# Kernel tuning notes

Measured on AMD Instinct MI355X. Metric: run time of the kernel, lower is better.

Reference implementation:

```python
import jax, jax.numpy as jnp
import numpy as np

EPS = 1e-8
NUM_ITER = 3
NUM_SLOTS = 8
NUM_HEADS = 4


def _ln(x, w, b):
    m = x.mean(-1, keepdims=True)
    v = x.var(-1, keepdims=True)
    return (x - m) / jnp.sqrt(v + 1e-5) * w + b


def setup_inputs() -> dict:
    key = jax.random.key(0)
    B, T, N, D, S, H = 16, 12, 1024, 256, 128, 256
    K = NUM_SLOTS
    ks = jax.random.split(key, 32)
    w = lambda i, shape: (0.02 * jax.random.normal(ks[i], shape)).astype(jnp.float32)
    f32 = jnp.float32
    return {
        'inputs': jax.random.normal(ks[0], (B, T, N, D), f32),
        'slots_noise': jax.random.normal(ks[1], (B, K, S), f32),
        'slot_mu': w(2, (1, 1, S)),
        'slot_log_sigma': w(3, (1, 1, S)),
        'ln_in_w': jnp.ones((D,), f32), 'ln_in_b': jnp.zeros((D,), f32),
        'ln_slots_w': jnp.ones((S,), f32), 'ln_slots_b': jnp.zeros((S,), f32),
        'ln_mlp_w': jnp.ones((S,), f32), 'ln_mlp_b': jnp.zeros((S,), f32),
        'Wq': w(4, (S, S)), 'Wk': w(5, (D, S)), 'Wv': w(6, (D, S)),
        'gru_Wih': w(7, (3 * S, S)), 'gru_Whh': w(8, (3 * S, S)),
        'gru_bih': jnp.zeros((3 * S,), f32), 'gru_bhh': jnp.zeros((3 * S,), f32),
        'mlp_W1': w(9, (S, H)), 'mlp_b1': jnp.zeros((H,), f32),
        'mlp_W2': w(10, (H, S)), 'mlp_b2': jnp.zeros((S,), f32),
        'p_ln1_w': jnp.ones((S,), f32), 'p_ln1_b': jnp.zeros((S,), f32),
        'p_Wq': w(11, (S, S)), 'p_Wk': w(12, (S, S)), 'p_Wv': w(13, (S, S)), 'p_Wo': w(14, (S, S)),
        'p_ln2_w': jnp.ones((S,), f32), 'p_ln2_b': jnp.zeros((S,), f32),
        'p_ffn_W1': w(15, (S, 4 * S)), 'p_ffn_b1': jnp.zeros((4 * S,), f32),
        'p_ffn_W2': w(16, (4 * S, S)), 'p_ffn_b2': jnp.zeros((S,), f32),
        'p_lnf_w': jnp.ones((S,), f32), 'p_lnf_b': jnp.zeros((S,), f32),
    }


def reference(inputs, slots_noise, slot_mu, slot_log_sigma,
              ln_in_w, ln_in_b, ln_slots_w, ln_slots_b, ln_mlp_w, ln_mlp_b,
              Wq, Wk, Wv, gru_Wih, gru_Whh, gru_bih, gru_bhh,
              mlp_W1, mlp_b1, mlp_W2, mlp_b2,
              p_ln1_w, p_ln1_b, p_Wq, p_Wk, p_Wv, p_Wo,
              p_ln2_w, p_ln2_b, p_ffn_W1, p_ffn_b1, p_ffn_W2, p_ffn_b2,
              p_lnf_w, p_lnf_b):
    B, T, N, D = inputs.shape
    S = slot_mu.shape[-1]
    K = NUM_SLOTS

    slots0 = slot_mu + jnp.exp(slot_log_sigma) * slots_noise  # (B,K,S)
    x = _ln(inputs, ln_in_w, ln_in_b)
    k = (x @ Wk) * (S ** -0.5)  # (B,T,N,S), pre-scaled keys
    v = x @ Wv                  # (B,T,N,S)

    def gru(u, h):  # torch GRUCell semantics; u,h: (B*K,S)
        gi = u @ gru_Wih.T + gru_bih
        gh = h @ gru_Whh.T + gru_bhh
        i_r, i_z, i_n = jnp.split(gi, 3, -1)
        h_r, h_z, h_n = jnp.split(gh, 3, -1)
        r = jax.nn.sigmoid(i_r + h_r)
        z = jax.nn.sigmoid(i_z + h_z)
        n = jnp.tanh(i_n + r * h_n)
        return (1.0 - z) * n + z * h

    def mha(y):  # (B,K,S) self-attention, pre-LN block style
        dh = S // NUM_HEADS
        split = lambda t: t.reshape(B, K, NUM_HEADS, dh).transpose(0, 2, 1, 3)
        q = split(y @ p_Wq) * (dh ** -0.5)
        kk = split(y @ p_Wk)
        vv = split(y @ p_Wv)
        a = jax.nn.softmax(jnp.einsum('bhqd,bhkd->bhqk', q, kk), -1)
        o = jnp.einsum('bhqk,bhkd->bhqd', a, vv).transpose(0, 2, 1, 3).reshape(B, K, S)
        return o @ p_Wo

    def predictor(s):
        s = s + mha(_ln(s, p_ln1_w, p_ln1_b))
        h = _ln(s, p_ln2_w, p_ln2_b)
        s = s + (jax.nn.relu(h @ p_ffn_W1 + p_ffn_b1) @ p_ffn_W2 + p_ffn_b2)
        return _ln(s, p_lnf_w, p_lnf_b)

    def step(slots, kv_t):
        k_t, v_t = kv_t  # (B,N,S) each
        attn_vis = None
        for i in range(NUM_ITER):
            slots_prev = slots
            q = _ln(slots, ln_slots_w, ln_slots_b) @ Wq          # (B,K,S)
            logits = jnp.einsum('bns,bks->bnk', k_t, q)           # (B,N,K)
            attn_vis = jax.nn.softmax(logits, -1)                 # over slots
            attn = attn_vis + EPS
            attn = attn / attn.sum(1, keepdims=True)              # normalize over inputs
            updates = jnp.einsum('bnk,bns->bks', attn, v_t)       # (B,K,S)
            slots = gru(updates.reshape(-1, S), slots_prev.reshape(-1, S)).reshape(B, K, S)
            if i < NUM_ITER - 1:
                h = _ln(slots, ln_mlp_w, ln_mlp_b)
                slots = slots + (jax.nn.relu(h @ mlp_W1 + mlp_b1) @ mlp_W2 + mlp_b2)
        return predictor(slots), (slots, attn_vis)

    kT = jnp.swapaxes(k, 0, 1)  # (T,B,N,S)
    vT = jnp.swapaxes(v, 0, 1)
    _, (slots_seq, attn_seq) = jax.lax.scan(step, slots0, (kT, vT))
    slots_collect = jnp.swapaxes(slots_seq, 0, 1)  # (B,T,K,S)
    attns_collect = jnp.swapaxes(attn_seq, 0, 1)   # (B,T,N,K)
    return slots_collect, attns_collect
```

## Files before the change

### kernel.cpp

```cpp
#include <hip/hip_runtime.h>
#include <hip/hip_bf16.h>

typedef _Float16 half8 __attribute__((ext_vector_type(8)));
typedef float floatx4 __attribute__((ext_vector_type(4)));

#define MFMA_F16(a, b, c) __builtin_amdgcn_mfma_f32_16x16x32_f16((a), (b), (c), 0, 0, 0)

__global__ void prep_w_kernel(const float* __restrict__ src, _Float16* __restrict__ dst,
                              int In, int Out, float scale, int doT) {
  int idx = blockIdx.x * 256 + threadIdx.x;
  if (idx >= In * Out) return;
  float v;
  if (doT) { int o = idx / In, i = idx - o * In; v = src[i * Out + o]; }
  else     { v = src[idx]; }
  dst[idx] = (_Float16)(v * scale);
}

__global__ void init_ctr_kernel(int* __restrict__ ctr) {
  if (threadIdx.x < 16) ctr[threadIdx.x] = 0;
}

__global__ __launch_bounds__(256) void gemm_kv_kernel(
    const float* __restrict__ x, const float* __restrict__ lnw_g,
    const float* __restrict__ lnb_g, const _Float16* __restrict__ WT,
    _Float16* __restrict__ kout, _Float16* __restrict__ vTout) {
  __shared__ union {
    struct { _Float16 A[128][72]; _Float16 B[128][72]; } s;
    _Float16 C[128][136];
  } u;
  __shared__ float s_mean[128], s_rstd[128], s_red[256][2], s_lnw[256], s_lnb[256];

  const int tid = threadIdx.x;
  const int bx = blockIdx.x, y = blockIdx.y;
  const size_t r0 = (size_t)bx * 128;
  const int w = tid >> 6, lane = tid & 63, quad = lane >> 4, l15 = lane & 15;

  s_lnw[tid] = lnw_g[tid];
  s_lnb[tid] = lnb_g[tid];
  {
    int row = tid >> 1, half = tid & 1;
    const float* p = x + (r0 + row) * 256 + half * 128;
    float s = 0.f, sq = 0.f;
    for (int i = 0; i < 32; i++) {
      float4 d = ((const float4*)p)[i];
      s += d.x + d.y + d.z + d.w;
      sq += d.x * d.x + d.y * d.y + d.z * d.z + d.w * d.w;
    }
    s_red[tid][0] = s; s_red[tid][1] = sq;
  }
  __syncthreads();
  if (tid < 128) {
    float s  = s_red[2 * tid][0] + s_red[2 * tid + 1][0];
    float sq = s_red[2 * tid][1] + s_red[2 * tid + 1][1];
    float m = s * (1.f / 256.f);
    float v = sq * (1.f / 256.f) - m * m;
    s_mean[tid] = m; s_rstd[tid] = rsqrtf(v + 1e-5f);
  }

  floatx4 acc[2][8];
  for (int rt = 0; rt < 2; rt++)
    for (int ct = 0; ct < 8; ct++) acc[rt][ct] = (floatx4){0.f, 0.f, 0.f, 0.f};

  for (int c = 0; c < 4; c++) {
    __syncthreads();
    for (int i = 0; i < 4; i++) {
      int g = tid + 256 * i;
      int row = g >> 3, c8 = g & 7;
      int col0 = c * 64 + c8 * 8;
      const float* p = x + (r0 + row) * 256 + col0;
      float4 d0 = ((const float4*)p)[0];
      float4 d1 = ((const float4*)p)[1];
      float f[8] = {d0.x, d0.y, d0.z, d0.w, d1.x, d1.y, d1.z, d1.w};
      float m = s_mean[row], rs = s_rstd[row];
      half8 hv;
      #pragma unroll
      for (int j = 0; j < 8; j++)
        hv[j] = (_Float16)((f[j] - m) * rs * s_lnw[col0 + j] + s_lnb[col0 + j]);
      *(half8*)&u.s.A[row][c8 * 8] = hv;
      *(half8*)&u.s.B[row][c8 * 8] = *(const half8*)(WT + (size_t)(y * 128 + row) * 256 + col0);
    }
    __syncthreads();
    #pragma unroll
    for (int ks = 0; ks < 2; ks++) {
      half8 af[2];
      af[0] = *(const half8*)&u.s.A[(2 * w) * 16 + l15][ks * 32 + quad * 8];
      af[1] = *(const half8*)&u.s.A[(2 * w + 1) * 16 + l15][ks * 32 + quad * 8];
      #pragma unroll
      for (int ct = 0; ct < 8; ct++) {
        half8 bf = *(const half8*)&u.s.B[ct * 16 + l15][ks * 32 + quad * 8];
        acc[0][ct] = MFMA_F16(af[0], bf, acc[0][ct]);
        acc[1][ct] = MFMA_F16(af[1], bf, acc[1][ct]);
      }
    }
  }

  const size_t bt = (size_t)(bx >> 3);
  const int n0loc = (bx & 7) * 128;
  if (y == 0) {
    for (int rt = 0; rt < 2; rt++)
      for (int ct = 0; ct < 8; ct++)
        #pragma unroll
        for (int r = 0; r < 4; r++) {
          size_t row = r0 + (2 * w + rt) * 16 + quad * 4 + r;
          kout[row * 128 + ct * 16 + l15] = (_Float16)acc[rt][ct][r];
        }
  } else {
    __syncthreads();
    for (int rt = 0; rt < 2; rt++)
      for (int ct = 0; ct < 8; ct++)
        #pragma unroll
        for (int r = 0; r < 4; r++)
          u.C[(2 * w + rt) * 16 + quad * 4 + r][ct * 16 + l15] = (_Float16)acc[rt][ct][r];
    __syncthreads();
    int s = tid >> 1, hf = tid & 1;
    for (int j = 0; j < 8; j++) {
      int nb = hf * 64 + j * 8;
      half8 tmp;
      #pragma unroll
      for (int e = 0; e < 8; e++) tmp[e] = u.C[nb + e][s];
      *(half8*)(vTout + (bt * 128 + s) * 1024 + n0loc + nb) = tmp;
    }
  }
}

struct P2Args {
  const _Float16 *kbuf, *vT;
  const _Float16 *WqT, *Wih, *Whh, *W1T, *W2T;
  const _Float16 *pQT, *pKT, *pVT, *pOT, *pF1T, *pF2T;
  const float *noise, *mu, *lsig;
  const float *lnsw, *lnsb, *lnmw, *lnmb;
  const float *bih, *bhh, *mb1, *mb2;
  const float *pl1w, *pl1b, *pl2w, *pl2b, *fb1, *fb2, *plfw, *plfb;
  float *out_slots, *out_attn;
  float *upd_p;
  float *col_p;
  float *vs_p;
  int   *ctr;
};

struct SH {
  _Float16 k_lds[128][136];
  _Float16 v_lds[128][136];
  float slots[8][128];
  _Float16 a16[16][136];
  _Float16 h16[16][136];
  union {
    struct { _Float16 qT[16][136]; _Float16 attnT[16][136]; } sa;
    struct { float gi[8][384]; float gh[8][384]; } gru;
    struct { _Float16 m16[16][264]; } mlp;
    struct { float qh[8][128]; float kh[8][128]; float vh[8][128]; float sc[4][8][8]; } mha;
    struct { _Float16 f16[16][520]; } ffn;
  } u;
  float colsum[8];
  float vsum[128];
  float bih[384], bhh[384], mb1[256], mb2[128], fb1[512], fb2[128];
  float lnsw[128], lnsb[128], lnmw[128], lnmb[128];
  float pl1w[128], pl1b[128], pl2w[128], pl2b[128], plfw[128], plfb[128];
};

__device__ __forceinline__ void group_barrier(int* ctr, int target) {
  __syncthreads();
  if (threadIdx.x == 0) {
    __hip_atomic_fetch_add(ctr, 1, __ATOMIC_ACQ_REL, __HIP_MEMORY_SCOPE_AGENT);
    while (__hip_atomic_load(ctr, __ATOMIC_ACQUIRE, __HIP_MEMORY_SCOPE_AGENT) < target)
      __builtin_amdgcn_s_sleep(1);
  }
  __syncthreads();
}

__device__ __forceinline__ void ln_to_a16(SH* sh, const float (*src)[128],
                                          const float* wv, const float* bv,
                                          int w, int lane) {
  if (w < 8) {
    float x0 = src[w][lane], x1 = src[w][lane + 64];
    float s = x0 + x1, sq = x0 * x0 + x1 * x1;
    #pragma unroll
    for (int m = 1; m < 64; m <<= 1) { s += __shfl_xor(s, m); sq += __shfl_xor(sq, m); }
    float mn = s * 0.0078125f;
    float vr = sq * 0.0078125f - mn * mn;
    float rs = rsqrtf(vr + 1e-5f);
    sh->a16[w][lane]      = (_Float16)((x0 - mn) * rs * wv[lane]      + bv[lane]);
    sh->a16[w][lane + 64] = (_Float16)((x1 - mn) * rs * wv[lane + 64] + bv[lane + 64]);
  } else {
    sh->a16[w][lane] = (_Float16)0.f;
    sh->a16[w][lane + 64] = (_Float16)0.f;
  }
}

__global__ __launch_bounds__(1024) void slot_attn_kernel(P2Args P) {
  __shared__ SH sh;
  const int tid = threadIdx.x;
  const int w = tid >> 6, lane = tid & 63, quad = lane >> 4, l15 = lane & 15;
  const int b = blockIdx.x & 15;
  const int g = blockIdx.x >> 4;
  const int n0 = g * 128;
  int* ctrb = P.ctr + b;
  int bar_phase = 0;

  for (int i = tid; i < 384; i += 1024) { sh.bih[i] = P.bih[i]; sh.bhh[i] = P.bhh[i]; }
  for (int i = tid; i < 256; i += 1024) sh.mb1[i] = P.mb1[i];
  for (int i = tid; i < 512; i += 1024) sh.fb1[i] = P.fb1[i];
  if (tid < 128) {
    sh.mb2[tid]  = P.mb2[tid];  sh.fb2[tid]  = P.fb2[tid];
    sh.lnsw[tid] = P.lnsw[tid]; sh.lnsb[tid] = P.lnsb[tid];
    sh.lnmw[tid] = P.lnmw[tid]; sh.lnmb[tid] = P.lnmb[tid];
    sh.pl1w[tid] = P.pl1w[tid]; sh.pl1b[tid] = P.pl1b[tid];
    sh.pl2w[tid] = P.pl2w[tid]; sh.pl2b[tid] = P.pl2b[tid];
    sh.plfw[tid] = P.plfw[tid]; sh.plfb[tid] = P.plfb[tid];
  }
  {
    int kk = tid >> 7, s = tid & 127;
    sh.slots[kk][s] = P.mu[s] + expf(P.lsig[s]) * P.noise[(b * 8 + kk) * 128 + s];
  }
  __syncthreads();

  for (int t = 0; t < 12; t++) {
    const _Float16* kt = P.kbuf + ((size_t)(b * 12 + t)) * 1024 * 128 + (size_t)n0 * 128;
    const _Float16* vt = P.vT   + ((size_t)(b * 12 + t)) * 128 * 1024 + n0;
    {
      int r = tid >> 4, c8 = (tid & 15) * 8;
      #pragma unroll
      for (int p = 0; p < 2; p++) {
        int row = p * 64 + r;
        *(half8*)&sh.k_lds[row][c8] = *(const half8*)(kt + (size_t)row * 128 + c8);
        *(half8*)&sh.v_lds[row][c8] = *(const half8*)(vt + (size_t)row * 1024 + c8);
      }
    }
    if (tid < 128) sh.vsum[tid] = 0.f;
    __syncthreads();
    {
      int s = tid >> 3, j = tid & 7;
      float a = 0.f;
      #pragma unroll
      for (int e = 0; e < 16; e++) a += (float)sh.v_lds[s][j * 16 + e];
      atomicAdd(&sh.vsum[s], a);
    }
    __syncthreads();
    if (tid < 128)
      __hip_atomic_store(&P.vs_p[(b * 8 + g) * 128 + tid], sh.vsum[tid],
                         __ATOMIC_RELAXED, __HIP_MEMORY_SCOPE_AGENT);

    for (int it = 0; it < 3; it++) {
      const int par = (t * 3 + it) & 1;
      float* updg = P.upd_p + ((size_t)(par * 16 + b) * 8 + g) * 1024;
      float* colg = P.col_p + ((size_t)(par * 16 + b) * 8 + g) * 8;
      if (w < 8) {
        float x0 = sh.slots[w][lane], x1 = sh.slots[w][lane + 64];
        sh.h16[w][lane] = (_Float16)x0; sh.h16[w][lane + 64] = (_Float16)x1;
        float s = x0 + x1, sq = x0 * x0 + x1 * x1;
        #pragma unroll
        for (int m = 1; m < 64; m <<= 1) { s += __shfl_xor(s, m); sq += __shfl_xor(sq, m); }
        float mn = s * 0.0078125f;
        float vr = sq * 0.0078125f - mn * mn;
        float rs = rsqrtf(vr + 1e-5f);
        sh.a16[w][lane]      = (_Float16)((x0 - mn) * rs * sh.lnsw[lane]      + sh.lnsb[lane]);
        sh.a16[w][lane + 64] = (_Float16)((x1 - mn) * rs * sh.lnsw[lane + 64] + sh.lnsb[lane + 64]);
      } else {
        sh.h16[w][lane] = (_Float16)0.f; sh.h16[w][lane + 64] = (_Float16)0.f;
        sh.a16[w][lane] = (_Float16)0.f; sh.a16[w][lane + 64] = (_Float16)0.f;
      }
      if (tid < 8) sh.colsum[tid] = 0.f;
      __syncthreads();
      if (w < 8) {
        floatx4 acc = (floatx4){0.f, 0.f, 0.f, 0.f};
        const _Float16* ar = &sh.a16[l15][quad * 8];
        const _Float16* br = P.WqT + (size_t)(w * 16 + l15) * 128 + quad * 8;
        #pragma unroll
        for (int ks = 0; ks < 4; ks++)
          acc = MFMA_F16(*(const half8*)(ar + ks * 32), *(const half8*)(br + ks * 32), acc);
        #pragma unroll
        for (int r = 0; r < 4; r++)
          sh.u.sa.qT[quad * 4 + r][w * 16 + l15] = (_Float16)acc[r];
      }
      __syncthreads();
      if (w < 8) {
        int nloc0 = w * 16;
        floatx4 acc = (floatx4){0.f, 0.f, 0.f, 0.f};
        const _Float16* ar = &sh.k_lds[nloc0 + l15][quad * 8];
        const _Float16* br = &sh.u.sa.qT[l15][quad * 8];
        #pragma unroll
        for (int ks = 0; ks < 4; ks++)
          acc = MFMA_F16(*(const half8*)(ar + ks * 32), *(const half8*)(br + ks * 32), acc);
        float cs = 0.f;
        #pragma unroll
        for (int r = 0; r < 4; r++) {
          float v = (l15 < 8) ? acc[r] : -3.0e38f;
          float mx = v;
          mx = fmaxf(mx, __shfl_xor(mx, 1, 16));
          mx = fmaxf(mx, __shfl_xor(mx, 2, 16));
          mx = fmaxf(mx, __shfl_xor(mx, 4, 16));
          mx = fmaxf(mx, __shfl_xor(mx, 8, 16));
          float pv = (l15 < 8) ? expf(v - mx) : 0.f;
          float ss = pv;
          ss += __shfl_xor(ss, 1, 16); ss += __shfl_xor(ss, 2, 16);
          ss += __shfl_xor(ss, 4, 16); ss += __shfl_xor(ss, 8, 16);
          float pn = pv / ss;
          cs += pn;
          int nloc = nloc0 + quad * 4 + r;
          sh.u.sa.attnT[l15][nloc] = (_Float16)pn;
          if (it == 2 && l15 < 8)
            P.out_attn[((size_t)(b * 12 + t) * 1024 + n0 + nloc) * 8 + l15] = pn;
        }
        cs += __shfl_xor(cs, 16); cs += __shfl_xor(cs, 32);
        if (lane < 8) atomicAdd(&sh.colsum[lane], cs);
      }
      __syncthreads();
      if (w < 8) {
        floatx4 acc = (floatx4){0.f, 0.f, 0.f, 0.f};
        const _Float16* ar = &sh.u.sa.attnT[l15][quad * 8];
        const _Float16* br = &sh.v_lds[w * 16 + l15][quad * 8];
        #pragma unroll
        for (int ks = 0; ks < 4; ks++)
          acc = MFMA_F16(*(const half8*)(ar + ks * 32), *(const half8*)(br + ks * 32), acc);
        int scol = w * 16 + l15;
        #pragma unroll
        for (int r = 0; r < 4; r++) {
          int slot = quad * 4 + r;
          if (slot < 8)
            __hip_atomic_store(&updg[slot * 128 + scol], acc[r],
                               __ATOMIC_RELAXED, __HIP_MEMORY_SCOPE_AGENT);
        }
      }
      if (tid < 8)
        __hip_atomic_store(&colg[tid], sh.colsum[tid],
                           __ATOMIC_RELAXED, __HIP_MEMORY_SCOPE_AGENT);
      bar_phase++;
      group_barrier(ctrb, 8 * bar_phase);
      {
        int slot = tid >> 7, scol = tid & 127;
        const float* up = P.upd_p + (size_t)(par * 16 + b) * 8 * 1024 + slot * 128 + scol;
        float sum = 0.f;
        #pragma unroll
        for (int gg = 0; gg < 8; gg++)
          sum += __hip_atomic_load((float*)(up + gg * 1024),
                                   __ATOMIC_RELAXED, __HIP_MEMORY_SCOPE_AGENT);
        float csum = 0.f;
        if (tid < 8) {
          const float* cp = P.col_p + (size_t)(par * 16 + b) * 8 * 8 + tid;
          #pragma unroll
          for (int gg = 0; gg < 8; gg++)
            csum += __hip_atomic_load((float*)(cp + gg * 8),
                                      __ATOMIC_RELAXED, __HIP_MEMORY_SCOPE_AGENT);
        }
        float vtot = 0.f;
        if (it == 0 && tid < 128) {
          const float* vp = P.vs_p + b * 8 * 128 + tid;
          #pragma unroll
          for (int gg = 0; gg < 8; gg++)
            vtot += __hip_atomic_load((float*)(vp + gg * 128),
                                      __ATOMIC_RELAXED, __HIP_MEMORY_SCOPE_AGENT);
        }
        __syncthreads();
        if (tid < 8) sh.colsum[tid] = csum;
        if (it == 0 && tid < 128) sh.vsum[tid] = vtot;
        __syncthreads();
        float upd = (sum + 1e-8f * sh.vsum[scol]) / (sh.colsum[slot] + 1024.f * 1e-8f);
        sh.a16[slot][scol] = (_Float16)upd;
        sh.a16[slot + 8][scol] = (_Float16)0.f;
      }
      __syncthreads();
      for (int j = w; j < 48; j += 16) {
        int isGi = (j < 24) ? 1 : 0;
        int ct = isGi ? j : j - 24;
        const _Float16* Ap = isGi ? &sh.a16[0][0] : &sh.h16[0][0];
        const _Float16* Bg = (isGi ? P.Wih : P.Whh) + (size_t)(ct * 16 + l15) * 128 + quad * 8;
        const _Float16* ar = Ap + l15 * 136 + quad * 8;
        floatx4 acc = (floatx4){0.f, 0.f, 0.f, 0.f};
        #pragma unroll
        for (int ks = 0; ks < 4; ks++)
          acc = MFMA_F16(*(const half8*)(ar + ks * 32), *(const half8*)(Bg + ks * 32), acc);
        int col = ct * 16 + l15;
        float bias = isGi ? sh.bih[col] : sh.bhh[col];
        float* dst = isGi ? &sh.u.gru.gi[0][0] : &sh.u.gru.gh[0][0];
        #pragma unroll
        for (int r = 0; r < 4; r++) {
          int slot = quad * 4 + r;
          if (slot < 8) dst[slot * 384 + col] = acc[r] + bias;
        }
      }
      __syncthreads();
      {
        int kk = tid >> 7, s = tid & 127;
        float gr = sh.u.gru.gi[kk][s]       + sh.u.gru.gh[kk][s];
        float gz = sh.u.gru.gi[kk][128 + s] + sh.u.gru.gh[kk][128 + s];
        float rg = 1.f / (1.f + expf(-gr));
        float zg = 1.f / (1.f + expf(-gz));
        float ng = tanhf(sh.u.gru.gi[kk][256 + s] + rg * sh.u.gru.gh[kk][256 + s]);
        float h = sh.slots[kk][s];
        sh.slots[kk][s] = (1.f - zg) * ng + zg * h;
      }
      __syncthreads();
      if (it < 2) {
        ln_to_a16(&sh, sh.slots, sh.lnmw, sh.lnmb, w, lane);
        __syncthreads();
        {
          floatx4 acc = (floatx4){0.f, 0.f, 0.f, 0.f};
          const _Float16* ar = &sh.a16[l15][quad * 8];
          const _Float16* br = P.W1T + (size_t)(w * 16 + l15) * 128 + quad * 8;
          #pragma unroll
          for (int ks = 0; ks < 4; ks++)
            acc = MFMA_F16(*(const half8*)(ar + ks * 32), *(const half8*)(br + ks * 32), acc);
          int col = w * 16 + l15;
          #pragma unroll
          for (int r = 0; r < 4; r++) {
            int slot = quad * 4 + r;
            if (slot < 8) sh.u.mlp.m16[slot][col] = (_Float16)fmaxf(acc[r] + sh.mb1[col], 0.f);
            else          sh.u.mlp.m16[slot][col] = (_Float16)0.f;
          }
        }
        __syncthreads();
        if (w < 8) {
          floatx4 acc = (floatx4){0.f, 0.f, 0.f, 0.f};
          const _Float16* ar = &sh.u.mlp.m16[l15][quad * 8];
          const _Float16* br = P.W2T + (size_t)(w * 16 + l15) * 256 + quad * 8;
          #pragma unroll
          for (int ks = 0; ks < 8; ks++)
            acc = MFMA_F16(*(const half8*)(ar + ks * 32), *(const half8*)(br + ks * 32), acc);
          int col = w * 16 + l15;
          #pragma unroll
          for (int r = 0; r < 4; r++) {
            int slot = quad * 4 + r;
            if (slot < 8) sh.slots[slot][col] += acc[r] + sh.mb2[col];
          }
        }
        __syncthreads();
      }
    }

    if (g == 0) {
      int kk = tid >> 7, s = tid & 127;
      P.out_slots[((size_t)(b * 12 + t) * 8 + kk) * 128 + s] = sh.slots[kk][s];
    }
    ln_to_a16(&sh, sh.slots, sh.pl1w, sh.pl1b, w, lane);
    __syncthreads();
    for (int j = w; j < 24; j += 16) {
      int gg = j >> 3, ct = j & 7;
      const _Float16* Bg = (gg == 0 ? P.pQT : (gg == 1 ? P.pKT : P.pVT)) + (size_t)(ct * 16 + l15) * 128 + quad * 8;
      const _Float16* ar = &sh.a16[l15][quad * 8];
      floatx4 acc = (floatx4){0.f, 0.f, 0.f, 0.f};
      #pragma unroll
      for (int ks = 0; ks < 4; ks++)
        acc = MFMA_F16(*(const half8*)(ar + ks * 32), *(const half8*)(Bg + ks * 32), acc);
      float scale = (gg == 0) ? 0.17677669529663687f : 1.f;
      float* dst = (gg == 0 ? &sh.u.mha.qh[0][0] : (gg == 1 ? &sh.u.mha.kh[0][0] : &sh.u.mha.vh[0][0]));
      int col = ct * 16 + l15;
      #pragma unroll
      for (int r = 0; r < 4; r++) {
        int slot = quad * 4 + r;
        if (slot < 8) dst[slot * 128 + col] = acc[r] * scale;
      }
    }
    __syncthreads();
    if (tid < 256) {
      int h = tid >> 6, a = (tid >> 3) & 7, b2 = tid & 7;
      const float* qr = &sh.u.mha.qh[a][h * 32];
      const float* kr = &sh.u.mha.kh[b2][h * 32];
      float s = 0.f;
      #pragma unroll
      for (int d = 0; d < 32; d++) s += qr[d] * kr[d];
      sh.u.mha.sc[h][a][b2] = s;
    }
    __syncthreads();
    if (tid < 32) {
      int h = tid >> 3, a = tid & 7;
      float* p = sh.u.mha.sc[h][a];
      float mx = p[0];
      #pragma unroll
      for (int j = 1; j < 8; j++) mx = fmaxf(mx, p[j]);
      float e[8]; float ssum = 0.f;
      #pragma unroll
      for (int j = 0; j < 8; j++) { e[j] = expf(p[j] - mx); ssum += e[j]; }
      float inv = 1.f / ssum;
      #pragma unroll
      for (int j = 0; j < 8; j++) p[j] = e[j] * inv;
    }
    __syncthreads();
    {
      int a = tid >> 7, col = tid & 127, h = col >> 5;
      float acc = 0.f;
      #pragma unroll
      for (int b2 = 0; b2 < 8; b2++) acc += sh.u.mha.sc[h][a][b2] * sh.u.mha.vh[b2][col];
      sh.a16[a][col] = (_Float16)acc;
    }
    __syncthreads();
    if (w < 8) {
      floatx4 acc = (floatx4){0.f, 0.f, 0.f, 0.f};
      const _Float16* ar = &sh.a16[l15][quad * 8];
      const _Float16* br = P.pOT + (size_t)(w * 16 + l15) * 128 + quad * 8;
      #pragma unroll
      for (int ks = 0; ks < 4; ks++)
        acc = MFMA_F16(*(const half8*)(ar + ks * 32), *(const half8*)(br + ks * 32), acc);
      int col = w * 16 + l15;
      #pragma unroll
      for (int r = 0; r < 4; r++) {
        int slot = quad * 4 + r;
        if (slot < 8) sh.slots[slot][col] += acc[r];
      }
    }
    __syncthreads();
    ln_to_a16(&sh, sh.slots, sh.pl2w, sh.pl2b, w, lane);
    __syncthreads();
    for (int ct = w; ct < 32; ct += 16) {
      floatx4 acc = (floatx4){0.f, 0.f, 0.f, 0.f};
      const _Float16* ar = &sh.a16[l15][quad * 8];
      const _Float16* br = P.pF1T + (size_t)(ct * 16 + l15) * 128 + quad * 8;
      #pragma unroll
      for (int ks = 0; ks < 4; ks++)
        acc = MFMA_F16(*(const half8*)(ar + ks * 32), *(const half8*)(br + ks * 32), acc);
      int col = ct * 16 + l15;
      #pragma unroll
      for (int r = 0; r < 4; r++) {
        int slot = quad * 4 + r;
        if (slot < 8) sh.u.ffn.f16[slot][col] = (_Float16)fmaxf(acc[r] + sh.fb1[col], 0.f);
        else          sh.u.ffn.f16[slot][col] = (_Float16)0.f;
      }
    }
    __syncthreads();
    if (w < 8) {
      floatx4 acc = (floatx4){0.f, 0.f, 0.f, 0.f};
      const _Float16* ar = &sh.u.ffn.f16[l15][quad * 8];
      const _Float16* br = P.pF2T + (size_t)(w * 16 + l15) * 512 + quad * 8;
      #pragma unroll 4
      for (int ks = 0; ks < 16; ks++)
        acc = MFMA_F16(*(const half8*)(ar + ks * 32), *(const half8*)(br + ks * 32), acc);
      int col = w * 16 + l15;
      #pragma unroll
      for (int r = 0; r < 4; r++) {
        int slot = quad * 4 + r;
        if (slot < 8) sh.slots[slot][col] += acc[r] + sh.fb2[col];
      }
    }
    __syncthreads();
    if (w < 8) {
      float x0 = sh.slots[w][lane], x1 = sh.slots[w][lane + 64];
      float s = x0 + x1, sq = x0 * x0 + x1 * x1;
      #pragma unroll
      for (int m = 1; m < 64; m <<= 1) { s += __shfl_xor(s, m); sq += __shfl_xor(sq, m); }
      float mn = s * 0.0078125f;
      float vr = sq * 0.0078125f - mn * mn;
      float rs = rsqrtf(vr + 1e-5f);
      sh.slots[w][lane]      = (x0 - mn) * rs * sh.plfw[lane]      + sh.plfb[lane];
      sh.slots[w][lane + 64] = (x1 - mn) * rs * sh.plfw[lane + 64] + sh.plfb[lane + 64];
    }
    __syncthreads();
  }
}

extern "C" void kernel_launch(void* const* d_in, const int* in_sizes, int n_in,
                              void* d_out, int out_size, void* d_ws, size_t ws_size,
                              hipStream_t stream) {
  const float* inp   = (const float*)d_in[0];
  const float* noise = (const float*)d_in[1];
  const float* mu    = (const float*)d_in[2];
  const float* lsig  = (const float*)d_in[3];
  const float* lniw  = (const float*)d_in[4];
  const float* lnib  = (const float*)d_in[5];
  const float* lnsw  = (const float*)d_in[6];
  const float* lnsb  = (const float*)d_in[7];
  const float* lnmw  = (const float*)d_in[8];
  const float* lnmb  = (const float*)d_in[9];
  const float* Wq    = (const float*)d_in[10];
  const float* Wk    = (const float*)d_in[11];
  const float* Wv    = (const float*)d_in[12];
  const float* gWih  = (const float*)d_in[13];
  const float* gWhh  = (const float*)d_in[14];
  const float* gbih  = (const float*)d_in[15];
  const float* gbhh  = (const float*)d_in[16];
  const float* mW1   = (const float*)d_in[17];
  const float* mb1   = (const float*)d_in[18];
  const float* mW2   = (const float*)d_in[19];
  const float* mb2   = (const float*)d_in[20];
  const float* pl1w  = (const float*)d_in[21];
  const float* pl1b  = (const float*)d_in[22];
  const float* pWq   = (const float*)d_in[23];
  const float* pWk   = (const float*)d_in[24];
  const float* pWv   = (const float*)d_in[25];
  const float* pWo   = (const float*)d_in[26];
  const float* pl2w  = (const float*)d_in[27];
  const float* pl2b  = (const float*)d_in[28];
  const float* pf1   = (const float*)d_in[29];
  const float* pfb1  = (const float*)d_in[30];
  const float* pf2   = (const float*)d_in[31];
  const float* pfb2  = (const float*)d_in[32];
  const float* plfw  = (const float*)d_in[33];
  const float* plfb  = (const float*)d_in[34];

  _Float16* p   = (_Float16*)d_ws;
  _Float16* kbuf = p;  p += 25165824;
  _Float16* vT   = p;  p += 25165824;
  _Float16* WT   = p;  p += 65536;
  _Float16* WqT  = p;  p += 16384;
  _Float16* Wih  = p;  p += 49152;
  _Float16* Whh  = p;  p += 49152;
  _Float16* W1T  = p;  p += 32768;
  _Float16* W2T  = p;  p += 32768;
  _Float16* pQT  = p;  p += 16384;
  _Float16* pKT  = p;  p += 16384;
  _Float16* pVT  = p;  p += 16384;
  _Float16* pOT  = p;  p += 16384;
  _Float16* pF1T = p;  p += 65536;
  _Float16* pF2T = p;  p += 65536;
  float* fb   = (float*)p;
  float* upd_p = fb;  fb += 2 * 16 * 8 * 1024;
  float* col_p = fb;  fb += 2 * 16 * 8 * 8;
  float* vs_p  = fb;  fb += 16 * 8 * 128;
  int*   ctr   = (int*)fb;

  const float kscale = 0.08838834764831845f;
  init_ctr_kernel<<<1, 64, 0, stream>>>(ctr);
  prep_w_kernel<<<128, 256, 0, stream>>>(Wk,   WT,         256, 128, kscale, 1);
  prep_w_kernel<<<128, 256, 0, stream>>>(Wv,   WT + 32768, 256, 128, 1.f,    1);
  prep_w_kernel<<<64,  256, 0, stream>>>(Wq,   WqT,        128, 128, 1.f,    1);
  prep_w_kernel<<<192, 256, 0, stream>>>(gWih, Wih,        49152, 1, 1.f,    0);
  prep_w_kernel<<<192, 256, 0, stream>>>(gWhh, Whh,        49152, 1, 1.f,    0);
  prep_w_kernel<<<128, 256, 0, stream>>>(mW1,  W1T,        128, 256, 1.f,    1);
  prep_w_kernel<<<128, 256, 0, stream>>>(mW2,  W2T,        256, 128, 1.f,    1);
  prep_w_kernel<<<64,  256, 0, stream>>>(pWq,  pQT,        128, 128, 1.f,    1);
  prep_w_kernel<<<64,  256, 0, stream>>>(pWk,  pKT,        128, 128, 1.f,    1);
  prep_w_kernel<<<64,  256, 0, stream>>>(pWv,  pVT,        128, 128, 1.f,    1);
  prep_w_kernel<<<64,  256, 0, stream>>>(pWo,  pOT,        128, 128, 1.f,    1);
  prep_w_kernel<<<256, 256, 0, stream>>>(pf1,  pF1T,       128, 512, 1.f,    1);
  prep_w_kernel<<<256, 256, 0, stream>>>(pf2,  pF2T,       512, 128, 1.f,    1);

  dim3 g1(1536, 2, 1);
  gemm_kv_kernel<<<g1, 256, 0, stream>>>(inp, lniw, lnib, WT, kbuf, vT);

  P2Args a;
  a.kbuf = kbuf; a.vT = vT;
  a.WqT = WqT; a.Wih = Wih; a.Whh = Whh; a.W1T = W1T; a.W2T = W2T;
  a.pQT = pQT; a.pKT = pKT; a.pVT = pVT; a.pOT = pOT; a.pF1T = pF1T; a.pF2T = pF2T;
  a.noise = noise; a.mu = mu; a.lsig = lsig;
  a.lnsw = lnsw; a.lnsb = lnsb; a.lnmw = lnmw; a.lnmb = lnmb;
  a.bih = gbih; a.bhh = gbhh; a.mb1 = mb1; a.mb2 = mb2;
  a.pl1w = pl1w; a.pl1b = pl1b; a.pl2w = pl2w; a.pl2b = pl2b;
  a.fb1 = pfb1; a.fb2 = pfb2; a.plfw = plfw; a.plfb = plfb;
  a.out_slots = (float*)d_out;
  a.out_attn  = (float*)d_out + 196608;
  a.upd_p = upd_p; a.col_p = col_p; a.vs_p = vs_p; a.ctr = ctr;

  slot_attn_kernel<<<128, 1024, 0, stream>>>(a);
}
```

Before: 1.370 ms.

## Overlap GRU hidden GEMM with attention, prefetch weight fragments, merge prep launches

Waves 8-15, idle during the attention phase, now compute the GRU hidden-state GEMM (Whh·h) early, so its input-side work runs alongside the slot attention. Weight fragments for Wq, Wih, W1, W2 and the predictor Q/K projections are loaded into registers ahead of the barriers that precede their use, hiding global latency. The GRU gate update is fused with the following LayerNorm into one per-wave pass, which removes a barrier and writes the output slots inline. The 13 weight-prep launches are merged into one 2D-grid kernel. Register pressure rises noticeably, and gi/gh move out of the shared-memory union, which enlarges shared memory.

```diff
diff --git a/kernel.cpp b/kernel.cpp
--- a/kernel.cpp
+++ b/kernel.cpp
@@ -6,14 +6,21 @@
 
 #define MFMA_F16(a, b, c) __builtin_amdgcn_mfma_f32_16x16x32_f16((a), (b), (c), 0, 0, 0)
 
-__global__ void prep_w_kernel(const float* __restrict__ src, _Float16* __restrict__ dst,
-                              int In, int Out, float scale, int doT) {
+struct PrepJobs {
+  const float* src[13];
+  _Float16* dst[13];
+  int In[13], Out[13], elems[13], doT[13];
+  float scale[13];
+};
+
+__global__ void prep_all_kernel(PrepJobs J) {
+  int j = blockIdx.y;
   int idx = blockIdx.x * 256 + threadIdx.x;
-  if (idx >= In * Out) return;
+  if (idx >= J.elems[j]) return;
   float v;
-  if (doT) { int o = idx / In, i = idx - o * In; v = src[i * Out + o]; }
-  else     { v = src[idx]; }
-  dst[idx] = (_Float16)(v * scale);
+  if (J.doT[j]) { int o = idx / J.In[j], i = idx - o * J.In[j]; v = J.src[j][i * J.Out[j] + o]; }
+  else          { v = J.src[j][idx]; }
+  J.dst[j][idx] = (_Float16)(v * J.scale[j]);
 }
 
 __global__ void init_ctr_kernel(int* __restrict__ ctr) {
@@ -144,9 +151,10 @@
   float slots[8][128];
   _Float16 a16[16][136];
   _Float16 h16[16][136];
+  float gi[8][384];
+  float gh[8][384];
   union {
     struct { _Float16 qT[16][136]; _Float16 attnT[16][136]; } sa;
-    struct { float gi[8][384]; float gh[8][384]; } gru;
     struct { _Float16 m16[16][264]; } mlp;
     struct { float qh[8][128]; float kh[8][128]; float vh[8][128]; float sc[4][8][8]; } mha;
     struct { _Float16 f16[16][520]; } ffn;
@@ -240,11 +248,19 @@
       __hip_atomic_store(&P.vs_p[(b * 8 + g) * 128 + tid], sh.vsum[tid],
                          __ATOMIC_RELAXED, __HIP_MEMORY_SCOPE_AGENT);
 
+    half8 qkvf[4];
+
     for (int it = 0; it < 3; it++) {
       const int par = (t * 3 + it) & 1;
       float* updg = P.upd_p + ((size_t)(par * 16 + b) * 8 + g) * 1024;
       float* colg = P.col_p + ((size_t)(par * 16 + b) * 8 + g) * 8;
+      half8 wqf[4], gif[4], w1f[4], w2f[8], whf[12];
       if (w < 8) {
+        {
+          const _Float16* br = P.WqT + (size_t)(w * 16 + l15) * 128 + quad * 8;
+          #pragma unroll
+          for (int ks = 0; ks < 4; ks++) wqf[ks] = *(const half8*)(br + ks * 32);
+        }
         float x0 = sh.slots[w][lane], x1 = sh.slots[w][lane + 64];
         sh.h16[w][lane] = (_Float16)x0; sh.h16[w][lane + 64] = (_Float16)x1;
         float s = x0 + x1, sq = x0 * x0 + x1 * x1;
@@ -264,15 +280,42 @@
       if (w < 8) {
         floatx4 acc = (floatx4){0.f, 0.f, 0.f, 0.f};
         const _Float16* ar = &sh.a16[l15][quad * 8];
-        const _Float16* br = P.WqT + (size_t)(w * 16 + l15) * 128 + quad * 8;
         #pragma unroll
         for (int ks = 0; ks < 4; ks++)
-          acc = MFMA_F16(*(const half8*)(ar + ks * 32), *(const half8*)(br + ks * 32), acc);
+          acc = MFMA_F16(*(const half8*)(ar + ks * 32), wqf[ks], acc);
         #pragma unroll
         for (int r = 0; r < 4; r++)
           sh.u.sa.qT[quad * 4 + r][w * 16 + l15] = (_Float16)acc[r];
+      } else {
+        const int idx8 = w - 8;
+        #pragma unroll
+        for (int tt = 0; tt < 3; tt++) {
+          int ct = idx8 + tt * 8;
+          const _Float16* Bg = P.Whh + (size_t)(ct * 16 + l15) * 128 + quad * 8;
+          #pragma unroll
+          for (int ks = 0; ks < 4; ks++) whf[tt * 4 + ks] = *(const half8*)(Bg + ks * 32);
+        }
+        #pragma unroll
+        for (int tt = 0; tt < 2; tt++) {
+          floatx4 acc = (floatx4){0.f, 0.f, 0.f, 0.f};
+          const _Float16* ar = &sh.h16[l15][quad * 8];
+          #pragma unroll
+          for (int ks = 0; ks < 4; ks++)
+            acc = MFMA_F16(*(const half8*)(ar + ks * 32), whf[tt * 4 + ks], acc);
+          int col = (idx8 + tt * 8) * 16 + l15;
+          #pragma unroll
+          for (int r = 0; r < 4; r++) {
+            int slot = quad * 4 + r;
+            if (slot < 8) sh.gh[slot][col] = acc[r] + sh.bhh[col];
+          }
+        }
       }
       __syncthreads();
+      {
+        const _Float16* Bg = P.Wih + (size_t)(w * 16 + l15) * 128 + quad * 8;
+        #pragma unroll
+        for (int ks = 0; ks < 4; ks++) gif[ks] = *(const half8*)(Bg + ks * 32);
+      }
       if (w < 8) {
         int nloc0 = w * 16;
         floatx4 acc = (floatx4){0.f, 0.f, 0.f, 0.f};
@@ -303,8 +346,26 @@
         }
         cs += __shfl_xor(cs, 16); cs += __shfl_xor(cs, 32);
         if (lane < 8) atomicAdd(&sh.colsum[lane], cs);
+      } else {
+        const int idx8 = w - 8;
+        floatx4 acc = (floatx4){0.f, 0.f, 0.f, 0.f};
+        const _Float16* ar = &sh.h16[l15][quad * 8];
+        #pragma unroll
+        for (int ks = 0; ks < 4; ks++)
+          acc = MFMA_F16(*(const half8*)(ar + ks * 32), whf[8 + ks], acc);
+        int col = (idx8 + 16) * 16 + l15;
+        #pragma unroll
+        for (int r = 0; r < 4; r++) {
+          int slot = quad * 4 + r;
+          if (slot < 8) sh.gh[slot][col] = acc[r] + sh.bhh[col];
+        }
       }
       __syncthreads();
+      if (it < 2) {
+        const _Float16* Bg = P.W1T + (size_t)(w * 16 + l15) * 128 + quad * 8;
+        #pragma unroll
+        for (int ks = 0; ks < 4; ks++) w1f[ks] = *(const half8*)(Bg + ks * 32);
+      }
       if (w < 8) {
         floatx4 acc = (floatx4){0.f, 0.f, 0.f, 0.f};
         const _Float16* ar = &sh.u.sa.attnT[l15][quad * 8];
@@ -356,50 +417,81 @@
         __syncthreads();
         float upd = (sum + 1e-8f * sh.vsum[scol]) / (sh.colsum[slot] + 1024.f * 1e-8f);
         sh.a16[slot][scol] = (_Float16)upd;
-        sh.a16[slot + 8][scol] = (_Float16)0.f;
       }
       __syncthreads();
-      for (int j = w; j < 48; j += 16) {
-        int isGi = (j < 24) ? 1 : 0;
-        int ct = isGi ? j : j - 24;
-        const _Float16* Ap = isGi ? &sh.a16[0][0] : &sh.h16[0][0];
-        const _Float16* Bg = (isGi ? P.Wih : P.Whh) + (size_t)(ct * 16 + l15) * 128 + quad * 8;
-        const _Float16* ar = Ap + l15 * 136 + quad * 8;
+      {
+        const _Float16* ar = &sh.a16[l15][quad * 8];
         floatx4 acc = (floatx4){0.f, 0.f, 0.f, 0.f};
         #pragma unroll
         for (int ks = 0; ks < 4; ks++)
-          acc = MFMA_F16(*(const half8*)(ar + ks * 32), *(const half8*)(Bg + ks * 32), acc);
-        int col = ct * 16 + l15;
-        float bias = isGi ? sh.bih[col] : sh.bhh[col];
-        float* dst = isGi ? &sh.u.gru.gi[0][0] : &sh.u.gru.gh[0][0];
+          acc = MFMA_F16(*(const half8*)(ar + ks * 32), gif[ks], acc);
+        int col = w * 16 + l15;
         #pragma unroll
         for (int r = 0; r < 4; r++) {
           int slot = quad * 4 + r;
-          if (slot < 8) dst[slot * 384 + col] = acc[r] + bias;
-        }
-      }
-      __syncthreads();
-      {
-        int kk = tid >> 7, s = tid & 127;
-        float gr = sh.u.gru.gi[kk][s]       + sh.u.gru.gh[kk][s];
-        float gz = sh.u.gru.gi[kk][128 + s] + sh.u.gru.gh[kk][128 + s];
-        float rg = 1.f / (1.f + expf(-gr));
-        float zg = 1.f / (1.f + expf(-gz));
-        float ng = tanhf(sh.u.gru.gi[kk][256 + s] + rg * sh.u.gru.gh[kk][256 + s]);
-        float h = sh.slots[kk][s];
-        sh.slots[kk][s] = (1.f - zg) * ng + zg * h;
+          if (slot < 8) sh.gi[slot][col] = acc[r] + sh.bih[col];
+        }
+        if (w < 8) {
+          int col2 = (16 + w) * 16 + l15;
+          const _Float16* Bg = P.Wih + (size_t)((16 + w) * 16 + l15) * 128 + quad * 8;
+          floatx4 acc2 = (floatx4){0.f, 0.f, 0.f, 0.f};
+          #pragma unroll
+          for (int ks = 0; ks < 4; ks++)
+            acc2 = MFMA_F16(*(const half8*)(ar + ks * 32), *(const half8*)(Bg + ks * 32), acc2);
+          #pragma unroll
+          for (int r = 0; r < 4; r++) {
+            int slot = quad * 4 + r;
+            if (slot < 8) sh.gi[slot][col2] = acc2[r] + sh.bih[col2];
+          }
+        }
       }
       __syncthreads();
       if (it < 2) {
-        ln_to_a16(&sh, sh.slots, sh.lnmw, sh.lnmb, w, lane);
-        __syncthreads();
+        if (w < 8) {
+          const _Float16* Bg = P.W2T + (size_t)(w * 16 + l15) * 256 + quad * 8;
+          #pragma unroll
+          for (int ks = 0; ks < 8; ks++) w2f[ks] = *(const half8*)(Bg + ks * 32);
+        }
+      } else {
+        const _Float16* Bg = ((w >> 3) == 0 ? P.pQT : P.pKT) + (size_t)((w & 7) * 16 + l15) * 128 + quad * 8;
+        #pragma unroll
+        for (int ks = 0; ks < 4; ks++) qkvf[ks] = *(const half8*)(Bg + ks * 32);
+      }
+      if (w < 8) {
+        float h0 = sh.slots[w][lane], h1 = sh.slots[w][lane + 64];
+        float r0 = 1.f / (1.f + expf(-(sh.gi[w][lane]       + sh.gh[w][lane])));
+        float z0 = 1.f / (1.f + expf(-(sh.gi[w][128 + lane] + sh.gh[w][128 + lane])));
+        float n0v = tanhf(sh.gi[w][256 + lane] + r0 * sh.gh[w][256 + lane]);
+        float x0 = (1.f - z0) * n0v + z0 * h0;
+        int l64 = lane + 64;
+        float r1 = 1.f / (1.f + expf(-(sh.gi[w][l64]       + sh.gh[w][l64])));
+        float z1 = 1.f / (1.f + expf(-(sh.gi[w][128 + l64] + sh.gh[w][128 + l64])));
+        float n1v = tanhf(sh.gi[w][256 + l64] + r1 * sh.gh[w][256 + l64]);
+        float x1 = (1.f - z1) * n1v + z1 * h1;
+        sh.slots[w][lane] = x0; sh.slots[w][lane + 64] = x1;
+        if (it == 2 && g == 0) {
+          P.out_slots[((size_t)(b * 12 + t) * 8 + w) * 128 + lane]      = x0;
+          P.out_slots[((size_t)(b * 12 + t) * 8 + w) * 128 + lane + 64] = x1;
+        }
+        const float* wv = (it < 2) ? sh.lnmw : sh.pl1w;
+        const float* bv = (it < 2) ? sh.lnmb : sh.pl1b;
+        float s = x0 + x1, sq = x0 * x0 + x1 * x1;
+        #pragma unroll
+        for (int m = 1; m < 64; m <<= 1) { s += __shfl_xor(s, m); sq += __shfl_xor(sq, m); }
+        float mn = s * 0.0078125f;
+        float vr = sq * 0.0078125f - mn * mn;
+        float rs = rsqrtf(vr + 1e-5f);
+        sh.a16[w][lane]      = (_Float16)((x0 - mn) * rs * wv[lane]      + bv[lane]);
+        sh.a16[w][lane + 64] = (_Float16)((x1 - mn) * rs * wv[lane + 64] + bv[lane + 64]);
+      }
+      __syncthreads();
+      if (it < 2) {
         {
           floatx4 acc = (floatx4){0.f, 0.f, 0.f, 0.f};
           const _Float16* ar = &sh.a16[l15][quad * 8];
-          const _Float16* br = P.W1T + (size_t)(w * 16 + l15) * 128 + quad * 8;
           #pragma unroll
           for (int ks = 0; ks < 4; ks++)
-            acc = MFMA_F16(*(const half8*)(ar + ks * 32), *(const half8*)(br + ks * 32), acc);
+            acc = MFMA_F16(*(const half8*)(ar + ks * 32), w1f[ks], acc);
           int col = w * 16 + l15;
           #pragma unroll
           for (int r = 0; r < 4; r++) {
@@ -412,10 +504,9 @@
         if (w < 8) {
           floatx4 acc = (floatx4){0.f, 0.f, 0.f, 0.f};
           const _Float16* ar = &sh.u.mlp.m16[l15][quad * 8];
-          const _Float16* br = P.W2T + (size_t)(w * 16 + l15) * 256 + quad * 8;
           #pragma unroll
           for (int ks = 0; ks < 8; ks++)
-            acc = MFMA_F16(*(const half8*)(ar + ks * 32), *(const half8*)(br + ks * 32), acc);
+            acc = MFMA_F16(*(const half8*)(ar + ks * 32), w2f[ks], acc);
           int col = w * 16 + l15;
           #pragma unroll
           for (int r = 0; r < 4; r++) {
@@ -427,27 +518,32 @@
       }
     }
 
-    if (g == 0) {
-      int kk = tid >> 7, s = tid & 127;
-      P.out_slots[((size_t)(b * 12 + t) * 8 + kk) * 128 + s] = sh.slots[kk][s];
-    }
-    ln_to_a16(&sh, sh.slots, sh.pl1w, sh.pl1b, w, lane);
-    __syncthreads();
-    for (int j = w; j < 24; j += 16) {
-      int gg = j >> 3, ct = j & 7;
-      const _Float16* Bg = (gg == 0 ? P.pQT : (gg == 1 ? P.pKT : P.pVT)) + (size_t)(ct * 16 + l15) * 128 + quad * 8;
+    {
       const _Float16* ar = &sh.a16[l15][quad * 8];
       floatx4 acc = (floatx4){0.f, 0.f, 0.f, 0.f};
       #pragma unroll
       for (int ks = 0; ks < 4; ks++)
-        acc = MFMA_F16(*(const half8*)(ar + ks * 32), *(const half8*)(Bg + ks * 32), acc);
+        acc = MFMA_F16(*(const half8*)(ar + ks * 32), qkvf[ks], acc);
+      int gg = w >> 3, ct = w & 7, col = ct * 16 + l15;
       float scale = (gg == 0) ? 0.17677669529663687f : 1.f;
-      float* dst = (gg == 0 ? &sh.u.mha.qh[0][0] : (gg == 1 ? &sh.u.mha.kh[0][0] : &sh.u.mha.vh[0][0]));
-      int col = ct * 16 + l15;
+      float* dst = (gg == 0) ? &sh.u.mha.qh[0][0] : &sh.u.mha.kh[0][0];
       #pragma unroll
       for (int r = 0; r < 4; r++) {
         int slot = quad * 4 + r;
         if (slot < 8) dst[slot * 128 + col] = acc[r] * scale;
+      }
+      if (w < 8) {
+        const _Float16* Bg = P.pVT + (size_t)(w * 16 + l15) * 128 + quad * 8;
+        floatx4 a2 = (floatx4){0.f, 0.f, 0.f, 0.f};
+        #pragma unroll
+        for (int ks = 0; ks < 4; ks++)
+          a2 = MFMA_F16(*(const half8*)(ar + ks * 32), *(const half8*)(Bg + ks * 32), a2);
+        int colv = w * 16 + l15;
+        #pragma unroll
+        for (int r = 0; r < 4; r++) {
+          int slot = quad * 4 + r;
+          if (slot < 8) sh.u.mha.vh[slot][colv] = a2[r];
+        }
       }
     }
     __syncthreads();
@@ -608,19 +704,21 @@
 
   const float kscale = 0.08838834764831845f;
   init_ctr_kernel<<<1, 64, 0, stream>>>(ctr);
-  prep_w_kernel<<<128, 256, 0, stream>>>(Wk,   WT,         256, 128, kscale, 1);
-  prep_w_kernel<<<128, 256, 0, stream>>>(Wv,   WT + 32768, 256, 128, 1.f,    1);
-  prep_w_kernel<<<64,  256, 0, stream>>>(Wq,   WqT,        128, 128, 1.f,    1);
-  prep_w_kernel<<<192, 256, 0, stream>>>(gWih, Wih,        49152, 1, 1.f,    0);
-  prep_w_kernel<<<192, 256, 0, stream>>>(gWhh, Whh,        49152, 1, 1.f,    0);
-  prep_w_kernel<<<128, 256, 0, stream>>>(mW1,  W1T,        128, 256, 1.f,    1);
-  prep_w_kernel<<<128, 256, 0, stream>>>(mW2,  W2T,        256, 128, 1.f,    1);
-  prep_w_kernel<<<64,  256, 0, stream>>>(pWq,  pQT,        128, 128, 1.f,    1);
-  prep_w_kernel<<<64,  256, 0, stream>>>(pWk,  pKT,        128, 128, 1.f,    1);
-  prep_w_kernel<<<64,  256, 0, stream>>>(pWv,  pVT,        128, 128, 1.f,    1);
-  prep_w_kernel<<<64,  256, 0, stream>>>(pWo,  pOT,        128, 128, 1.f,    1);
-  prep_w_kernel<<<256, 256, 0, stream>>>(pf1,  pF1T,       128, 512, 1.f,    1);
-  prep_w_kernel<<<256, 256, 0, stream>>>(pf2,  pF2T,       512, 128, 1.f,    1);
+
+  PrepJobs J;
+  const float* srcs[13] = {Wk, Wv, Wq, gWih, gWhh, mW1, mW2, pWq, pWk, pWv, pWo, pf1, pf2};
+  _Float16* dsts[13]    = {WT, WT + 32768, WqT, Wih, Whh, W1T, W2T, pQT, pKT, pVT, pOT, pF1T, pF2T};
+  int Ins[13]    = {256, 256, 128, 49152, 49152, 128, 256, 128, 128, 128, 128, 128, 512};
+  int Outs[13]   = {128, 128, 128, 1, 1, 256, 128, 128, 128, 128, 128, 512, 128};
+  int elemss[13] = {32768, 32768, 16384, 49152, 49152, 32768, 32768, 16384, 16384, 16384, 16384, 65536, 65536};
+  int doTs[13]   = {1, 1, 1, 0, 0, 1, 1, 1, 1, 1, 1, 1, 1};
+  float scales[13] = {kscale, 1.f, 1.f, 1.f, 1.f, 1.f, 1.f, 1.f, 1.f, 1.f, 1.f, 1.f, 1.f};
+  for (int j = 0; j < 13; j++) {
+    J.src[j] = srcs[j]; J.dst[j] = dsts[j]; J.In[j] = Ins[j]; J.Out[j] = Outs[j];
+    J.elems[j] = elemss[j]; J.doT[j] = doTs[j]; J.scale[j] = scales[j];
+  }
+  dim3 gp(256, 13, 1);
+  prep_all_kernel<<<gp, 256, 0, stream>>>(J);
 
   dim3 g1(1536, 2, 1);
   gemm_kv_kernel<<<g1, 256, 0, stream>>>(inp, lniw, lnib, WT, kbuf, vT);
```

Measured after the change: 1.768 ms. 1.29x slower.
